# Performance work log

Hardware: AMD Instinct MI355X
Metric: run time of the kernel (lower is better)

The kernel has to match this reference:

```python
import jax, jax.numpy as jnp
import numpy as np

B, S, D = 1024, 200, 512
D_FF = 256


def setup_inputs() -> dict:
    key = jax.random.key(0)
    ks = jax.random.split(key, 8)
    s = 0.02  # init scale to keep gates in a sane range
    return {
        "target": jax.random.normal(ks[0], (B, D), jnp.float32),
        "history": jax.random.normal(ks[1], (B, S, D), jnp.float32),
        "W_ih": jax.random.normal(ks[2], (3 * D, D), jnp.float32) * s,
        "W_hh": jax.random.normal(ks[3], (3 * D, D), jnp.float32) * s,
        "b_ih": jnp.zeros((3 * D,), jnp.float32),
        "b_hh": jnp.zeros((3 * D,), jnp.float32),
        "W_fc": jax.random.normal(ks[4], (D_FF, 2 * D), jnp.float32) * s,
        "b_fc": jnp.zeros((D_FF,), jnp.float32),
        "W_sc": jax.random.normal(ks[5], (1, D_FF), jnp.float32) * s,
        "b_sc": jnp.zeros((1,), jnp.float32),
    }


def _gru(history, W_ih, W_hh, b_ih, b_hh):
    # Precompute input-side gate pre-activations for all steps: [B, S, 3D]
    gx = jnp.einsum("bsd,gd->bsg", history, W_ih) + b_ih
    d = history.shape[-1]
    h0 = jnp.zeros((history.shape[0], d), history.dtype)

    def step(h, gx_t):
        gh = h @ W_hh.T + b_hh  # [B, 3D]
        xr, xz, xn = jnp.split(gx_t, 3, axis=-1)
        hr, hz, hn = jnp.split(gh, 3, axis=-1)
        r = jax.nn.sigmoid(xr + hr)
        z = jax.nn.sigmoid(xz + hz)
        n = jnp.tanh(xn + r * hn)
        h_new = (1.0 - z) * n + z * h
        return h_new, h_new

    _, out = jax.lax.scan(step, h0, jnp.swapaxes(gx, 0, 1))  # out: [S, B, D]
    return jnp.swapaxes(out, 0, 1)  # [B, S, D]


def reference(target, history, W_ih, W_hh, b_ih, b_hh, W_fc, b_fc, W_sc, b_sc):
    d = target.shape[-1]
    gru_out = _gru(history, W_ih, W_hh, b_ih, b_hh)  # [B, S, D]

    # concat([gru_out, target]) @ W_fc.T  == gru_out @ Wg.T + target @ Wt.T
    Wg, Wt = W_fc[:, :d], W_fc[:, d:]
    pre = jnp.einsum("bsd,fd->bsf", gru_out, Wg) + (target @ Wt.T)[:, None, :] + b_fc
    hidden = jax.nn.gelu(pre, approximate=False)  # torch F.gelu default is exact erf
    scores = jnp.einsum("bsf,f->bs", hidden, W_sc[0]) + b_sc[0]  # [B, S]
    w = jax.nn.softmax(scores, axis=-1)
    interest = jnp.einsum("bs,bsd->bd", w, gru_out)  # [B, D]
    return jnp.concatenate([interest, target], axis=-1)  # [B, 2D]
```

## Files before the change

kernel.cpp:

```cpp
#include <hip/hip_runtime.h>

typedef __attribute__((ext_vector_type(8))) short short8v;
typedef __attribute__((ext_vector_type(4))) float f32x4;

#define NB 1024
#define NS 200
#define ND 512
#define NG 1536
#define NM 204800
#define NFF 256

#define GRU_P 4
#define GRU_G 64

__device__ __forceinline__ float bf2f(unsigned short u){
  union { unsigned u; float f; } v; v.u = ((unsigned)u) << 16; return v.f;
}
__device__ __forceinline__ unsigned short f2bf(float f){
  union { float f; unsigned u; } v; v.f = f;
  unsigned r = v.u + 0x7fffu + ((v.u >> 16) & 1u);
  return (unsigned short)(r >> 16);
}
__device__ __forceinline__ float sigm(float x){ return 1.f / (1.f + __expf(-x)); }
__device__ __forceinline__ float tanhfast(float x){ return 1.f - 2.f / (1.f + __expf(2.f * x)); }

__global__ void k_prepack(const float* __restrict__ W, unsigned short* __restrict__ out,
                          int ld, int coloff, int ntiles){
  int gid = blockIdx.x * 256 + threadIdx.x;
  if (gid >= ntiles * 1024) return;
  int ntile = gid >> 10; int rem = gid & 1023;
  int kk = rem >> 6; int lane = rem & 63;
  int c = ntile * 16 + (lane & 15);
  int k0 = kk * 32 + (lane >> 4) * 8;
  const float* s = W + (size_t)c * ld + coloff + k0;
  uint4 v;
  v.x = (unsigned)f2bf(s[0]) | ((unsigned)f2bf(s[1]) << 16);
  v.y = (unsigned)f2bf(s[2]) | ((unsigned)f2bf(s[3]) << 16);
  v.z = (unsigned)f2bf(s[4]) | ((unsigned)f2bf(s[5]) << 16);
  v.w = (unsigned)f2bf(s[6]) | ((unsigned)f2bf(s[7]) << 16);
  *(uint4*)(out + (size_t)gid * 8) = v;
}

__global__ void k_tvec(const float* __restrict__ target, const float* __restrict__ Wfc,
                       const float* __restrict__ bfc, float* __restrict__ tvec){
  __shared__ float tg[4][ND];
  int bb = blockIdx.x;
  int tid = threadIdx.x;
  for (int idx = tid; idx < 4 * ND; idx += 256){
    int j = idx >> 9, d = idx & 511;
    tg[j][d] = target[(size_t)(bb * 4 + j) * ND + d];
  }
  __syncthreads();
  const float* wrow = Wfc + (size_t)tid * 1024 + 512;
  float a0 = 0, a1 = 0, a2 = 0, a3 = 0;
  for (int d = 0; d < ND; ++d){
    float wv = wrow[d];
    a0 += tg[0][d] * wv; a1 += tg[1][d] * wv; a2 += tg[2][d] * wv; a3 += tg[3][d] * wv;
  }
  float bias = bfc[tid];
  tvec[(size_t)(bb * 4 + 0) * NFF + tid] = a0 + bias;
  tvec[(size_t)(bb * 4 + 1) * NFF + tid] = a1 + bias;
  tvec[(size_t)(bb * 4 + 2) * NFF + tid] = a2 + bias;
  tvec[(size_t)(bb * 4 + 3) * NFF + tid] = a3 + bias;
}

__global__ __launch_bounds__(256) void k_gemm_gx(const float* __restrict__ Af,
                                                 const unsigned short* __restrict__ Bpk,
                                                 const float* __restrict__ bih,
                                                 const float* __restrict__ bhh,
                                                 unsigned short* __restrict__ gx){
  __shared__ unsigned short As[128 * 64];
  int tid = threadIdx.x; int lane = tid & 63; int wid = tid >> 6;
  int wm = wid >> 1, wn = wid & 1;
  int Nb = blockIdx.x, Mb = blockIdx.y;
  const float* Abase = Af + (size_t)Mb * 128 * ND;
  const short8v* Bp = (const short8v*)Bpk;
  f32x4 acc[4][4];
  #pragma unroll
  for (int i = 0; i < 4; ++i)
    #pragma unroll
    for (int j = 0; j < 4; ++j) acc[i][j] = (f32x4){0.f, 0.f, 0.f, 0.f};

  for (int kc = 0; kc < 8; ++kc){
    __syncthreads();
    #pragma unroll
    for (int pass = 0; pass < 4; ++pass){
      int idx = pass * 256 + tid; int r = idx >> 3, ch = idx & 7;
      const float* src = Abase + (size_t)r * ND + kc * 64 + ch * 8;
      float4 f0 = *(const float4*)src;
      float4 f1 = *(const float4*)(src + 4);
      uint4 v;
      v.x = (unsigned)f2bf(f0.x) | ((unsigned)f2bf(f0.y) << 16);
      v.y = (unsigned)f2bf(f0.z) | ((unsigned)f2bf(f0.w) << 16);
      v.z = (unsigned)f2bf(f1.x) | ((unsigned)f2bf(f1.y) << 16);
      v.w = (unsigned)f2bf(f1.z) | ((unsigned)f2bf(f1.w) << 16);
      *(uint4*)&As[r * 64 + ch * 8] = v;
    }
    __syncthreads();
    #pragma unroll
    for (int i = 0; i < 2; ++i){
      short8v a[4];
      #pragma unroll
      for (int mt = 0; mt < 4; ++mt)
        a[mt] = *(const short8v*)&As[(wm * 64 + mt * 16 + (lane & 15)) * 64 + i * 32 + (lane >> 4) * 8];
      #pragma unroll
      for (int nt = 0; nt < 4; ++nt){
        short8v b = Bp[((size_t)(Nb * 8 + wn * 4 + nt) * 16 + (kc * 2 + i)) * 64 + lane];
        #pragma unroll
        for (int mt = 0; mt < 4; ++mt)
          acc[mt][nt] = __builtin_amdgcn_mfma_f32_16x16x32_bf16(a[mt], b, acc[mt][nt], 0, 0, 0);
      }
    }
  }
  #pragma unroll
  for (int mt = 0; mt < 4; ++mt){
    #pragma unroll
    for (int nt = 0; nt < 4; ++nt){
      int gcol = Nb * 128 + wn * 64 + nt * 16 + (lane & 15);
      float bv = bih[gcol] + (gcol < 1024 ? bhh[gcol] : 0.f);
      #pragma unroll
      for (int r = 0; r < 4; ++r){
        int grow = Mb * 128 + wm * 64 + mt * 16 + (lane >> 4) * 4 + r;
        gx[(size_t)grow * NG + gcol] = f2bf(acc[mt][nt][r] + bv);
      }
    }
  }
}

__global__ __launch_bounds__(512, 1) void k_gru11(const unsigned short* __restrict__ gx,
                                                  const unsigned short* __restrict__ Wpk,
                                                  const float* __restrict__ bhh,
                                                  unsigned short* __restrict__ gout,
                                                  unsigned long long* __restrict__ hx,
                                                  int* __restrict__ flags){
  __shared__ unsigned short hbuf[2][16 * 512];
  __shared__ unsigned short hstg[16][136];
  int tid = threadIdx.x; int lane = tid & 63; int nh = tid >> 6;
  int bid = blockIdx.x; int g = bid & 63; int s = bid >> 6;
  int colg = lane & 15;
  int rowg = lane >> 4;
  int c_h = s * 128 + nh * 16 + colg;
  int b0 = g * 16;
  int* gfl = flags + g * 32;

  for (int i = tid; i < 16 * 512; i += 512) hbuf[0][i] = 0;

  short8v wf[3][16];
  const short8v* Wp = (const short8v*)Wpk;
  #pragma unroll
  for (int gg = 0; gg < 3; ++gg){
    int ntile = gg * 32 + s * 8 + nh;
    #pragma unroll
    for (int kk = 0; kk < 16; ++kk)
      wf[gg][kk] = Wp[((size_t)ntile * 16 + kk) * 64 + lane];
  }
  float bN = bhh[1024 + c_h];
  float hreg[4] = {0.f, 0.f, 0.f, 0.f};

  int wbat = tid >> 5;
  int wc4  = tid & 31;

  unsigned short cxr[4], cxz[4], cxn[4];
  #pragma unroll
  for (int r = 0; r < 4; ++r){
    const unsigned short* gp = gx + ((size_t)(b0 + rowg * 4 + r) * NS + 0) * NG;
    cxr[r] = gp[c_h]; cxz[r] = gp[512 + c_h]; cxn[r] = gp[1024 + c_h];
  }
  __syncthreads();

  #pragma unroll 1
  for (int t = 0; t < NS; ++t){
    int par = t & 1;
    const unsigned short* hr = hbuf[par];
    f32x4 acc0 = (f32x4){0.f,0.f,0.f,0.f}, acc1 = acc0, acc2 = acc0;
    #pragma unroll
    for (int kc = 0; kc < 16; ++kc){
      short8v a = *(const short8v*)&hr[kc * 512 + lane * 8];
      acc0 = __builtin_amdgcn_mfma_f32_16x16x32_bf16(a, wf[0][kc], acc0, 0, 0, 0);
      acc1 = __builtin_amdgcn_mfma_f32_16x16x32_bf16(a, wf[1][kc], acc1, 0, 0, 0);
      acc2 = __builtin_amdgcn_mfma_f32_16x16x32_bf16(a, wf[2][kc], acc2, 0, 0, 0);
    }
    unsigned short hnew[4];
    #pragma unroll
    for (int r = 0; r < 4; ++r){
      float rr = sigm(bf2f(cxr[r]) + acc0[r]);
      float zz = sigm(bf2f(cxz[r]) + acc1[r]);
      float nn = tanhfast(bf2f(cxn[r]) + rr * (acc2[r] + bN));
      float h = nn + zz * (hreg[r] - nn);
      hreg[r] = h;
      hnew[r] = f2bf(h);
    }

    if (t + 1 < NS){
      unsigned long long* hxp = hx + (size_t)par * (1024 * 128);
      #pragma unroll
      for (int r = 0; r < 4; ++r) hstg[rowg * 4 + r][nh * 16 + colg] = hnew[r];
      __syncthreads();
      {
        unsigned long long v8 = *(const unsigned long long*)&hstg[wbat][wc4 * 4];
        __hip_atomic_store(&hxp[(size_t)(b0 + wbat) * 128 + s * 32 + wc4], v8,
                           __ATOMIC_RELAXED, __HIP_MEMORY_SCOPE_AGENT);
      }
      asm volatile("s_waitcnt vmcnt(0)" ::: "memory");
      if (lane == 0)
        __hip_atomic_store(&gfl[s * 8 + nh], t + 1, __ATOMIC_RELAXED, __HIP_MEMORY_SCOPE_AGENT);
      #pragma unroll
      for (int r = 0; r < 4; ++r)
        gout[((size_t)(b0 + rowg * 4 + r) * NS + t) * ND + c_h] = hnew[r];
      #pragma unroll
      for (int r = 0; r < 4; ++r){
        const unsigned short* gp = gx + ((size_t)(b0 + rowg * 4 + r) * NS + (t + 1)) * NG;
        cxr[r] = gp[c_h]; cxz[r] = gp[512 + c_h]; cxn[r] = gp[1024 + c_h];
      }
      {
        int need = t + 1; int fv;
        for (;;){
          fv = (lane < 32) ? __hip_atomic_load(&gfl[lane], __ATOMIC_RELAXED, __HIP_MEMORY_SCOPE_AGENT) : need;
          if (__all(fv >= need)) break;
          __builtin_amdgcn_s_sleep(2);
        }
      }
      asm volatile("" ::: "memory");
      unsigned short* hw = hbuf[par ^ 1];
      #pragma unroll
      for (int q = 0; q < 2; ++q){
        int kc = q * 8 + nh;
        size_t base = (size_t)(b0 + (lane & 15)) * 128 + kc * 8 + (lane >> 4) * 2;
        unsigned long long u0 = __hip_atomic_load(&hxp[base],     __ATOMIC_RELAXED, __HIP_MEMORY_SCOPE_AGENT);
        unsigned long long u1 = __hip_atomic_load(&hxp[base + 1], __ATOMIC_RELAXED, __HIP_MEMORY_SCOPE_AGENT);
        unsigned long long tmp[2] = {u0, u1};
        *(uint4*)&hw[kc * 512 + lane * 8] = *(const uint4*)tmp;
      }
      __syncthreads();
    } else {
      #pragma unroll
      for (int r = 0; r < 4; ++r)
        gout[((size_t)(b0 + rowg * 4 + r) * NS + t) * ND + c_h] = hnew[r];
    }
  }
}

__global__ __launch_bounds__(512) void k_gemm_s4(const unsigned short* __restrict__ A,
                                                 const unsigned short* __restrict__ Bpk,
                                                 const float* __restrict__ tvec,
                                                 const float* __restrict__ Wsc,
                                                 const float* __restrict__ bsc,
                                                 float* __restrict__ scores){
  __shared__ unsigned short As[128 * 64];
  __shared__ float spart[4][128];
  int tid = threadIdx.x; int lane = tid & 63; int wid = tid >> 6;
  int wm = wid >> 2, wn = wid & 3;
  int Mb = blockIdx.x;
  const unsigned short* Abase = A + (size_t)Mb * 128 * ND;
  const short8v* Bp = (const short8v*)Bpk;
  f32x4 acc[4][4];
  #pragma unroll
  for (int i = 0; i < 4; ++i)
    #pragma unroll
    for (int j = 0; j < 4; ++j) acc[i][j] = (f32x4){0.f, 0.f, 0.f, 0.f};

  for (int kc = 0; kc < 8; ++kc){
    __syncthreads();
    #pragma unroll
    for (int pass = 0; pass < 2; ++pass){
      int idx = pass * 512 + tid; int r = idx >> 3, ch = idx & 7;
      uint4 v = *(const uint4*)(Abase + (size_t)r * ND + kc * 64 + ch * 8);
      *(uint4*)&As[r * 64 + ch * 8] = v;
    }
    __syncthreads();
    #pragma unroll
    for (int i = 0; i < 2; ++i){
      short8v a[4];
      #pragma unroll
      for (int mt = 0; mt < 4; ++mt)
        a[mt] = *(const short8v*)&As[(wm * 64 + mt * 16 + (lane & 15)) * 64 + i * 32 + (lane >> 4) * 8];
      #pragma unroll
      for (int nt = 0; nt < 4; ++nt){
        short8v b = Bp[((size_t)(wn * 4 + nt) * 16 + (kc * 2 + i)) * 64 + lane];
        #pragma unroll
        for (int mt = 0; mt < 4; ++mt)
          acc[mt][nt] = __builtin_amdgcn_mfma_f32_16x16x32_bf16(a[mt], b, acc[mt][nt], 0, 0, 0);
      }
    }
  }
  #pragma unroll
  for (int mt = 0; mt < 4; ++mt){
    #pragma unroll
    for (int r = 0; r < 4; ++r){
      int rowl = wm * 64 + mt * 16 + (lane >> 4) * 4 + r;
      unsigned grow = (unsigned)(Mb * 128 + rowl);
      unsigned bidx = grow / 200u;
      float rowsum = 0.f;
      #pragma unroll
      for (int nt = 0; nt < 4; ++nt){
        int gcol = wn * 64 + nt * 16 + (lane & 15);
        float pre = acc[mt][nt][r] + tvec[(size_t)bidx * NFF + gcol];
        float g = 0.5f * pre * (1.f + erff(pre * 0.70710678118654752f));
        rowsum += g * Wsc[gcol];
      }
      rowsum += __shfl_xor(rowsum, 1, 64);
      rowsum += __shfl_xor(rowsum, 2, 64);
      rowsum += __shfl_xor(rowsum, 4, 64);
      rowsum += __shfl_xor(rowsum, 8, 64);
      if ((lane & 15) == 0) spart[wn][rowl] = rowsum;
    }
  }
  __syncthreads();
  if (tid < 128){
    float s = spart[0][tid] + spart[1][tid] + spart[2][tid] + spart[3][tid] + bsc[0];
    scores[(size_t)Mb * 128 + tid] = s;
  }
}

__global__ void k_out(const float* __restrict__ scores, const unsigned short* __restrict__ gout,
                      const float* __restrict__ target, float* __restrict__ out){
  int b = blockIdx.x; int tid = threadIdx.x;
  __shared__ float sw[NS];
  __shared__ float red[4];
  float v = (tid < NS) ? scores[(size_t)b * NS + tid] : -3.0e38f;
  float m = v;
  #pragma unroll
  for (int off = 32; off >= 1; off >>= 1) m = fmaxf(m, __shfl_xor(m, off, 64));
  if ((tid & 63) == 0) red[tid >> 6] = m;
  __syncthreads();
  m = fmaxf(fmaxf(red[0], red[1]), fmaxf(red[2], red[3]));
  float e = (tid < NS) ? __expf(v - m) : 0.f;
  if (tid < NS) sw[tid] = e;
  float su = e;
  #pragma unroll
  for (int off = 32; off >= 1; off >>= 1) su += __shfl_xor(su, off, 64);
  __syncthreads();
  if ((tid & 63) == 0) red[tid >> 6] = su;
  __syncthreads();
  float inv = 1.f / (red[0] + red[1] + red[2] + red[3]);
  int d0 = tid * 2;
  float a0 = 0.f, a1 = 0.f;
  const unsigned short* gbase = gout + (size_t)b * NS * ND + d0;
  for (int s = 0; s < NS; ++s){
    unsigned u = *(const unsigned*)(gbase + (size_t)s * ND);
    float wgt = sw[s];
    a0 += wgt * bf2f((unsigned short)(u & 0xffffu));
    a1 += wgt * bf2f((unsigned short)(u >> 16));
  }
  out[(size_t)b * 1024 + d0] = a0 * inv;
  out[(size_t)b * 1024 + d0 + 1] = a1 * inv;
  float2 tv = *(const float2*)(target + (size_t)b * ND + d0);
  out[(size_t)b * 1024 + 512 + d0] = tv.x;
  out[(size_t)b * 1024 + 512 + d0 + 1] = tv.y;
}

extern "C" void kernel_launch(void* const* d_in, const int* in_sizes, int n_in,
                              void* d_out, int out_size, void* d_ws, size_t ws_size,
                              hipStream_t stream) {
  const float* target  = (const float*)d_in[0];
  const float* history = (const float*)d_in[1];
  const float* W_ih    = (const float*)d_in[2];
  const float* W_hh    = (const float*)d_in[3];
  const float* b_ih    = (const float*)d_in[4];
  const float* b_hh    = (const float*)d_in[5];
  const float* W_fc    = (const float*)d_in[6];
  const float* b_fc    = (const float*)d_in[7];
  const float* W_sc    = (const float*)d_in[8];
  const float* b_sc    = (const float*)d_in[9];

  char* ws = (char*)d_ws;
  size_t off = 0;
  unsigned short* gx     = (unsigned short*)(ws + off); off += 629145600ull;
  unsigned short* gout   = (unsigned short*)(ws + off); off += 209715200ull;
  unsigned short* wih_pk = (unsigned short*)(ws + off); off += 1572864ull;
  unsigned short* whh_pk = (unsigned short*)(ws + off); off += 1572864ull;
  unsigned short* wg_pk  = (unsigned short*)(ws + off); off += 262144ull;
  float*          tvec   = (float*)(ws + off);          off += 1048576ull;
  float*          scores = (float*)(ws + off);          off += 819200ull;
  unsigned long long* hx = (unsigned long long*)(ws + off); off += 2097152ull;
  int*            flags  = (int*)(ws + off);             off += 8192ull;
  if (ws_size < off) return;
  float* outp = (float*)d_out;

  (void)hipMemsetAsync(flags, 0, GRU_G * 32 * sizeof(int), stream);
  k_prepack<<<384, 256, 0, stream>>>(W_ih, wih_pk, 512, 0, 96);
  k_prepack<<<384, 256, 0, stream>>>(W_hh, whh_pk, 512, 0, 96);
  k_prepack<<<64, 256, 0, stream>>>(W_fc, wg_pk, 1024, 0, 16);
  k_tvec<<<256, 256, 0, stream>>>(target, W_fc, b_fc, tvec);
  k_gemm_gx<<<dim3(12, 1600), 256, 0, stream>>>(history, wih_pk, b_ih, b_hh, gx);
  k_gru11<<<256, 512, 0, stream>>>(gx, whh_pk, b_hh, gout, hx, flags);
  k_gemm_s4<<<1600, 512, 0, stream>>>(gout, wg_pk, tvec, W_sc, b_sc, scores);
  k_out<<<1024, 256, 0, stream>>>(scores, gout, target, outp);
}
```

Before: 2.293 ms.

## Halve GRU block to 4 waves, each computing two column tiles per gate

The persistent GRU recurrence kernel now uses 256 threads per block instead of 512. Each wave holds two 16-column tiles of W_hh per gate (six MFMA accumulators) in registers, so each shared A-fragment load feeds twice as many MFMAs. Flag polling now covers 16 per-wave flags instead of 32, and the s_sleep in the spin loop is removed so waiters react faster. In exchange, register pressure roughly doubles from the weight fragments, with some risk of spills, and fewer waves per CU are left to hide latency.

```diff
diff --git a/kernel.cpp b/kernel.cpp
--- a/kernel.cpp
+++ b/kernel.cpp
@@ -127,7 +127,7 @@
   }
 }
 
-__global__ __launch_bounds__(512, 1) void k_gru11(const unsigned short* __restrict__ gx,
+__global__ __launch_bounds__(256, 1) void k_gru12(const unsigned short* __restrict__ gx,
                                                   const unsigned short* __restrict__ Wpk,
                                                   const float* __restrict__ bhh,
                                                   unsigned short* __restrict__ gout,
@@ -135,36 +135,44 @@
                                                   int* __restrict__ flags){
   __shared__ unsigned short hbuf[2][16 * 512];
   __shared__ unsigned short hstg[16][136];
-  int tid = threadIdx.x; int lane = tid & 63; int nh = tid >> 6;
+  int tid = threadIdx.x; int lane = tid & 63; int w = tid >> 6;
   int bid = blockIdx.x; int g = bid & 63; int s = bid >> 6;
   int colg = lane & 15;
   int rowg = lane >> 4;
-  int c_h = s * 128 + nh * 16 + colg;
+  int c0 = s * 128 + w * 32 + colg;
+  int c1 = c0 + 16;
   int b0 = g * 16;
-  int* gfl = flags + g * 32;
-
-  for (int i = tid; i < 16 * 512; i += 512) hbuf[0][i] = 0;
-
-  short8v wf[3][16];
+  int* gfl = flags + g * 16;
+
+  for (int i = tid; i < 16 * 512; i += 256) hbuf[0][i] = 0;
+
+  short8v wf[6][16];
   const short8v* Wp = (const short8v*)Wpk;
   #pragma unroll
-  for (int gg = 0; gg < 3; ++gg){
-    int ntile = gg * 32 + s * 8 + nh;
-    #pragma unroll
-    for (int kk = 0; kk < 16; ++kk)
-      wf[gg][kk] = Wp[((size_t)ntile * 16 + kk) * 64 + lane];
-  }
-  float bN = bhh[1024 + c_h];
-  float hreg[4] = {0.f, 0.f, 0.f, 0.f};
-
-  int wbat = tid >> 5;
-  int wc4  = tid & 31;
-
-  unsigned short cxr[4], cxz[4], cxn[4];
+  for (int gg = 0; gg < 3; ++gg)
+    #pragma unroll
+    for (int j = 0; j < 2; ++j){
+      int ntile = gg * 32 + s * 8 + w * 2 + j;
+      #pragma unroll
+      for (int kk = 0; kk < 16; ++kk)
+        wf[gg * 2 + j][kk] = Wp[((size_t)ntile * 16 + kk) * 64 + lane];
+    }
+  float bN0 = bhh[1024 + c0], bN1 = bhh[1024 + c1];
+  float hreg[2][4];
+  #pragma unroll
+  for (int j = 0; j < 2; ++j)
+    #pragma unroll
+    for (int r = 0; r < 4; ++r) hreg[j][r] = 0.f;
+
+  int wbat = tid >> 4;
+  int wc2  = (tid & 15) * 2;
+
+  unsigned short cxr[2][4], cxz[2][4], cxn[2][4];
   #pragma unroll
   for (int r = 0; r < 4; ++r){
     const unsigned short* gp = gx + ((size_t)(b0 + rowg * 4 + r) * NS + 0) * NG;
-    cxr[r] = gp[c_h]; cxz[r] = gp[512 + c_h]; cxn[r] = gp[1024 + c_h];
+    cxr[0][r] = gp[c0]; cxz[0][r] = gp[512 + c0]; cxn[0][r] = gp[1024 + c0];
+    cxr[1][r] = gp[c1]; cxz[1][r] = gp[512 + c1]; cxn[1][r] = gp[1024 + c1];
   }
   __syncthreads();
 
@@ -172,60 +180,73 @@
   for (int t = 0; t < NS; ++t){
     int par = t & 1;
     const unsigned short* hr = hbuf[par];
-    f32x4 acc0 = (f32x4){0.f,0.f,0.f,0.f}, acc1 = acc0, acc2 = acc0;
+    f32x4 acc[6];
+    #pragma unroll
+    for (int nt = 0; nt < 6; ++nt) acc[nt] = (f32x4){0.f, 0.f, 0.f, 0.f};
     #pragma unroll
     for (int kc = 0; kc < 16; ++kc){
       short8v a = *(const short8v*)&hr[kc * 512 + lane * 8];
-      acc0 = __builtin_amdgcn_mfma_f32_16x16x32_bf16(a, wf[0][kc], acc0, 0, 0, 0);
-      acc1 = __builtin_amdgcn_mfma_f32_16x16x32_bf16(a, wf[1][kc], acc1, 0, 0, 0);
-      acc2 = __builtin_amdgcn_mfma_f32_16x16x32_bf16(a, wf[2][kc], acc2, 0, 0, 0);
-    }
-    unsigned short hnew[4];
-    #pragma unroll
-    for (int r = 0; r < 4; ++r){
-      float rr = sigm(bf2f(cxr[r]) + acc0[r]);
-      float zz = sigm(bf2f(cxz[r]) + acc1[r]);
-      float nn = tanhfast(bf2f(cxn[r]) + rr * (acc2[r] + bN));
-      float h = nn + zz * (hreg[r] - nn);
-      hreg[r] = h;
-      hnew[r] = f2bf(h);
+      #pragma unroll
+      for (int nt = 0; nt < 6; ++nt)
+        acc[nt] = __builtin_amdgcn_mfma_f32_16x16x32_bf16(a, wf[nt][kc], acc[nt], 0, 0, 0);
+    }
+    unsigned short hnew[2][4];
+    #pragma unroll
+    for (int j = 0; j < 2; ++j){
+      float bN = j ? bN1 : bN0;
+      #pragma unroll
+      for (int r = 0; r < 4; ++r){
+        float rr = sigm(bf2f(cxr[j][r]) + acc[j][r]);
+        float zz = sigm(bf2f(cxz[j][r]) + acc[2 + j][r]);
+        float nn = tanhfast(bf2f(cxn[j][r]) + rr * (acc[4 + j][r] + bN));
+        float h = nn + zz * (hreg[j][r] - nn);
+        hreg[j][r] = h;
+        hnew[j][r] = f2bf(h);
+      }
     }
 
     if (t + 1 < NS){
       unsigned long long* hxp = hx + (size_t)par * (1024 * 128);
       #pragma unroll
-      for (int r = 0; r < 4; ++r) hstg[rowg * 4 + r][nh * 16 + colg] = hnew[r];
+      for (int j = 0; j < 2; ++j)
+        #pragma unroll
+        for (int r = 0; r < 4; ++r)
+          hstg[rowg * 4 + r][w * 32 + j * 16 + colg] = hnew[j][r];
       __syncthreads();
       {
-        unsigned long long v8 = *(const unsigned long long*)&hstg[wbat][wc4 * 4];
-        __hip_atomic_store(&hxp[(size_t)(b0 + wbat) * 128 + s * 32 + wc4], v8,
+        unsigned long long v0 = *(const unsigned long long*)&hstg[wbat][wc2 * 4];
+        unsigned long long v1 = *(const unsigned long long*)&hstg[wbat][wc2 * 4 + 4];
+        __hip_atomic_store(&hxp[(size_t)(b0 + wbat) * 128 + s * 32 + wc2], v0,
+                           __ATOMIC_RELAXED, __HIP_MEMORY_SCOPE_AGENT);
+        __hip_atomic_store(&hxp[(size_t)(b0 + wbat) * 128 + s * 32 + wc2 + 1], v1,
                            __ATOMIC_RELAXED, __HIP_MEMORY_SCOPE_AGENT);
       }
       asm volatile("s_waitcnt vmcnt(0)" ::: "memory");
       if (lane == 0)
-        __hip_atomic_store(&gfl[s * 8 + nh], t + 1, __ATOMIC_RELAXED, __HIP_MEMORY_SCOPE_AGENT);
-      #pragma unroll
-      for (int r = 0; r < 4; ++r)
-        gout[((size_t)(b0 + rowg * 4 + r) * NS + t) * ND + c_h] = hnew[r];
+        __hip_atomic_store(&gfl[s * 4 + w], t + 1, __ATOMIC_RELAXED, __HIP_MEMORY_SCOPE_AGENT);
+      #pragma unroll
+      for (int r = 0; r < 4; ++r){
+        unsigned short* gp = gout + ((size_t)(b0 + rowg * 4 + r) * NS + t) * ND;
+        gp[c0] = hnew[0][r]; gp[c1] = hnew[1][r];
+      }
       #pragma unroll
       for (int r = 0; r < 4; ++r){
         const unsigned short* gp = gx + ((size_t)(b0 + rowg * 4 + r) * NS + (t + 1)) * NG;
-        cxr[r] = gp[c_h]; cxz[r] = gp[512 + c_h]; cxn[r] = gp[1024 + c_h];
+        cxr[0][r] = gp[c0]; cxz[0][r] = gp[512 + c0]; cxn[0][r] = gp[1024 + c0];
+        cxr[1][r] = gp[c1]; cxz[1][r] = gp[512 + c1]; cxn[1][r] = gp[1024 + c1];
       }
       {
         int need = t + 1; int fv;
-        for (;;){
-          fv = (lane < 32) ? __hip_atomic_load(&gfl[lane], __ATOMIC_RELAXED, __HIP_MEMORY_SCOPE_AGENT) : need;
-          if (__all(fv >= need)) break;
-          __builtin_amdgcn_s_sleep(2);
-        }
+        do {
+          fv = (lane < 16) ? __hip_atomic_load(&gfl[lane], __ATOMIC_RELAXED, __HIP_MEMORY_SCOPE_AGENT) : need;
+        } while (!__all(fv >= need));
       }
       asm volatile("" ::: "memory");
       unsigned short* hw = hbuf[par ^ 1];
       #pragma unroll
-      for (int q = 0; q < 2; ++q){
-        int kc = q * 8 + nh;
-        size_t base = (size_t)(b0 + (lane & 15)) * 128 + kc * 8 + (lane >> 4) * 2;
+      for (int q = 0; q < 4; ++q){
+        int kc = w * 4 + q;
+        size_t base = (size_t)(b0 + colg) * 128 + kc * 8 + rowg * 2;
         unsigned long long u0 = __hip_atomic_load(&hxp[base],     __ATOMIC_RELAXED, __HIP_MEMORY_SCOPE_AGENT);
         unsigned long long u1 = __hip_atomic_load(&hxp[base + 1], __ATOMIC_RELAXED, __HIP_MEMORY_SCOPE_AGENT);
         unsigned long long tmp[2] = {u0, u1};
@@ -234,8 +255,10 @@
       __syncthreads();
     } else {
       #pragma unroll
-      for (int r = 0; r < 4; ++r)
-        gout[((size_t)(b0 + rowg * 4 + r) * NS + t) * ND + c_h] = hnew[r];
+      for (int r = 0; r < 4; ++r){
+        unsigned short* gp = gout + ((size_t)(b0 + rowg * 4 + r) * NS + t) * ND;
+        gp[c0] = hnew[0][r]; gp[c1] = hnew[1][r];
+      }
     }
   }
 }
@@ -373,17 +396,17 @@
   float*          tvec   = (float*)(ws + off);          off += 1048576ull;
   float*          scores = (float*)(ws + off);          off += 819200ull;
   unsigned long long* hx = (unsigned long long*)(ws + off); off += 2097152ull;
-  int*            flags  = (int*)(ws + off);             off += 8192ull;
+  int*            flags  = (int*)(ws + off);             off += 4096ull;
   if (ws_size < off) return;
   float* outp = (float*)d_out;
 
-  (void)hipMemsetAsync(flags, 0, GRU_G * 32 * sizeof(int), stream);
+  (void)hipMemsetAsync(flags, 0, GRU_G * 16 * sizeof(int), stream);
   k_prepack<<<384, 256, 0, stream>>>(W_ih, wih_pk, 512, 0, 96);
   k_prepack<<<384, 256, 0, stream>>>(W_hh, whh_pk, 512, 0, 96);
   k_prepack<<<64, 256, 0, stream>>>(W_fc, wg_pk, 1024, 0, 16);
   k_tvec<<<256, 256, 0, stream>>>(target, W_fc, b_fc, tvec);
   k_gemm_gx<<<dim3(12, 1600), 256, 0, stream>>>(history, wih_pk, b_ih, b_hh, gx);
-  k_gru11<<<256, 512, 0, stream>>>(gx, whh_pk, b_hh, gout, hx, flags);
+  k_gru12<<<256, 256, 0, stream>>>(gx, whh_pk, b_hh, gout, hx, flags);
   k_gemm_s4<<<1600, 512, 0, stream>>>(gout, wg_pk, tvec, W_sc, b_sc, scores);
   k_out<<<1024, 256, 0, stream>>>(scores, gout, target, outp);
 }
```

New measurement: 2.084 ms. 9.1% less time.
